# Optimization experiments

Hardware: AMD Instinct MI355X
Metric: run time of the kernel (lower is better)

Reference implementation:

```python
import jax, jax.numpy as jnp
import numpy as np

N_BINS = 50
FEATURE_ID = 0
EPS = 1e-7  # keras backend epsilon used by binary_crossentropy clipping


def setup_inputs() -> dict:
    key = jax.random.key(0)
    k1, k2 = jax.random.split(key)
    inputs = jax.random.normal(k1, (8_000_000, 4), dtype=jnp.float32)
    targets = jax.random.randint(k2, (8_000_000,), 0, 2, dtype=jnp.int32)
    return {"inputs": inputs, "targets": targets}


def _cut_forward(inputs, targets):
    # x: selected feature column, y: binary labels
    x = inputs[:, FEATURE_ID]
    y = targets
    N = x.shape[0]
    n_f = jnp.float32(N)

    x_min = jnp.min(x)
    x_max = jnp.max(x)
    E = N_BINS + 1
    edges = jnp.linspace(x_min, x_max, E)

    # Sort events once; prefix-sum of signal labels gives exact class counts
    # below/above any threshold (equivalent to the per-bin compare+count loop,
    # including the original's inclusive [lower, upper] double-counting of edges).
    order = jnp.argsort(x)
    xs = x[order]
    ys = (y[order] == 1).astype(jnp.float32)
    cs = jnp.concatenate([jnp.zeros((1,), jnp.float32), jnp.cumsum(ys)])  # [N+1]
    Ns = cs[-1]
    Nb = n_f - Ns

    r = jnp.searchsorted(xs, edges, side='right')  # count(x <= e)
    l = jnp.searchsorted(xs, edges, side='left')   # count(x <  e)
    ns_le = cs[r]
    ns_lt = cs[l]
    nb_le = r.astype(jnp.float32) - ns_le
    nb_lt = l.astype(jnp.float32) - ns_lt

    # hist[i] = count(lower[i] <= v <= upper[i]) per class
    hist0 = nb_le[1:] - nb_lt[:-1]  # background, [N_BINS]
    hist1 = ns_le[1:] - ns_lt[:-1]  # signal

    # candidate bin edges: sign-flip boundaries of hist0>hist1 with non-empty bins
    gt0 = hist0 > hist1
    cand0 = jnp.logical_xor(gt0[:-1], gt0[1:]) & (hist0[:-1] > 0)
    gt1 = hist1 > hist0
    cand1 = jnp.logical_xor(gt1[:-1], gt1[1:]) & (hist1[:-1] > 0)
    mask = jnp.zeros((E,), bool).at[1:N_BINS].set(cand0 | cand1)
    cnt = jnp.sum(mask)
    # original appends x_max when exactly one candidate survives
    mask = mask.at[-1].set(mask[-1] | (cnt == 1))

    # clipped BCE on hard 0/1 predictions reduces to a weighted error count:
    # correct sample -> -log(1-eps), wrong sample -> -log(eps)
    a = -jnp.log1p(jnp.float32(-EPS))
    b = -jnp.log(jnp.float32(EPS))

    def bce(correct):
        return ((n_f - correct) * b + correct * a) / n_f

    # per-edge losses for single-threshold cases
    c0 = ns_le + (Nb - nb_le)          # case 0: pred = (x <= c)
    c1 = (Ns - ns_lt) + nb_lt          # case 1: pred = (x >= c)
    # per-pair losses (i = lower cut, j = upper cut)
    c2 = (ns_le[None, :] - ns_lt[:, None]) + Nb - (nb_le[None, :] - nb_lt[:, None])
    c3 = ns_le[:, None] + (Ns - ns_lt[None, :]) + (nb_le[None, :] - nb_lt[:, None])

    L = jnp.stack([
        jnp.broadcast_to(bce(c0)[:, None], (E, E)),
        jnp.broadcast_to(bce(c1)[:, None], (E, E)),
        bce(c2),
        bce(c3),
    ])  # [4, E, E]
    per_pair_min = jnp.min(L, axis=0)
    per_pair_case = jnp.argmin(L, axis=0)

    idx = jnp.arange(E)
    valid = mask[:, None] & mask[None, :] & (idx[:, None] < idx[None, :])
    flat = jnp.argmin(jnp.where(valid, per_pair_min, jnp.inf))
    i = flat // E
    j = flat % E
    lower = edges[i]
    upper = edges[j]
    case = per_pair_case[i, j]

    pred0 = x <= lower
    pred1 = x >= lower
    pred2 = pred1 & (x <= upper)
    pred3 = pred0 | (x >= upper)
    y_pred = jnp.where(case == 0, pred0,
             jnp.where(case == 1, pred1,
             jnp.where(case == 2, pred2, pred3)))
    return y_pred


def reference(inputs, targets):
    return _cut_forward(inputs, targets).astype(jnp.int32)
```

## Files before the change

### kernel.cpp

```cpp
#include <hip/hip_runtime.h>
#include <math.h>
#include <stdint.h>

#define N_BINS 50
#define EDGE_N 51
#define HIST_N 52
#define NTHR 256
#define MAXBLK 2048
#define NREP 16

typedef unsigned int u32;
typedef unsigned short u16;
typedef unsigned char u8;
typedef float f32x4 __attribute__((ext_vector_type(4)));


#define KEEP16(v) asm volatile("" :: "v"(v))
#define ALOAD(p)     __hip_atomic_load((p), __ATOMIC_RELAXED, __HIP_MEMORY_SCOPE_AGENT)
#define ASTORE(p, v) __hip_atomic_store((p), (v), __ATOMIC_RELAXED, __HIP_MEMORY_SCOPE_AGENT)
#define AADD(p, v)   __hip_atomic_fetch_add((p), (v), __ATOMIC_RELAXED, __HIP_MEMORY_SCOPE_AGENT)
#define VDRAIN() asm volatile("s_waitcnt vmcnt(0)" ::: "memory")

__device__ __forceinline__ u32 f32_enc(float f) {
  u32 u = __float_as_uint(f);
  return (u & 0x80000000u) ? ~u : (u | 0x80000000u);
}
__device__ __forceinline__ float f32_dec(u32 k) {
  u32 u = (k & 0x80000000u) ? (k & 0x7fffffffu) : ~k;
  return __uint_as_float(u);
}
__device__ __forceinline__ u32* slot(u32* wsu, int base_b, int i) {
  return (u32*)((char*)wsu + base_b + i * 64);
}

__device__ __forceinline__ float edge_at(int e, float xmin, float xmax) {
  if (e >= N_BINS) return xmax;
  float step = __fdiv_rn((float)e, (float)N_BINS);
  float omst = __fsub_rn(1.0f, step);
  return __fadd_rn(__fmul_rn(xmin, omst), __fmul_rn(xmax, step));
}

__device__ __forceinline__ float bce_f(int c, float n_f, float aC, float bC) {
  float cf = (float)c;
  float t = __fadd_rn(__fmul_rn(__fsub_rn(n_f, cf), bC), __fmul_rn(cf, aC));
  return __fdiv_rn(t, n_f);
}

__device__ __forceinline__ void get_ab(float& aC, float& bC) {
  const double epsd = (double)1e-7f;
  aC = (float)(-log1p(-epsd));
  bC = (float)(-log(epsd));
}

__global__ void k_init(u32* __restrict__ wsu) {
  const int t = threadIdx.x;
  for (int i = t; i < 21376 / 4; i += NTHR) wsu[i] = 0u;
}

template <int COMPACT>
__global__ void __launch_bounds__(NTHR, 8)
k_all(const f32x4* __restrict__ in4, const int* __restrict__ tgt, int n, int nblk,
      u32* __restrict__ wsu, int* __restrict__ histU, int* __restrict__ histE,
      u32* __restrict__ bminArr, u32* __restrict__ bmaxArr,
      u8* __restrict__ codes, float* __restrict__ xc, int* __restrict__ out) {
  __shared__ int shU[2 * HIST_N];
  __shared__ float s_edges[EDGE_N];
  __shared__ int shE[2 * EDGE_N];
  __shared__ float s_red[8];
  __shared__ u32 s_redu[8];
  __shared__ float s_mm[2];
  __shared__ int s_ns_le[EDGE_N], s_ns_lt[EDGE_N], s_nb_le[EDGE_N], s_nb_lt[EDGE_N];
  __shared__ int s_h0[N_BINS], s_h1[N_BINS];
  __shared__ unsigned char s_g0[N_BINS], s_g1[N_BINS];
  __shared__ unsigned char s_mask[EDGE_N];
  __shared__ float s_rv[NTHR];
  __shared__ int s_ri[NTHR];
  __shared__ int s_cut[3];

  const int tid = threadIdx.x, bid = blockIdx.x;
  const int gid = bid * NTHR + tid;
  const int T = nblk * NTHR;
  const int rep = bid & (NREP - 1);

  for (int i = tid; i < 2 * HIST_N; i += NTHR) shU[i] = 0;
  for (int i = tid; i < 2 * EDGE_N; i += NTHR) shE[i] = 0;

  float vmin = INFINITY, vmax = -INFINITY;
#pragma unroll 4
  for (int i = gid; i < n; i += T) {
    f32x4 r = in4[i];
    KEEP16(r);
    float x = r.x;
    vmin = fminf(vmin, x);
    vmax = fmaxf(vmax, x);
    if (COMPACT) xc[i] = x;
  }
  for (int off = 32; off; off >>= 1) {
    vmin = fminf(vmin, __shfl_down(vmin, off));
    vmax = fmaxf(vmax, __shfl_down(vmax, off));
  }
  {
    int wid = tid >> 6;
    if ((tid & 63) == 0) { s_red[wid] = vmin; s_red[4 + wid] = vmax; }
  }
  __syncthreads();
  if (tid == 0) {
    float m = s_red[0], M = s_red[4];
    for (int w = 1; w < NTHR / 64; ++w) { m = fminf(m, s_red[w]); M = fmaxf(M, s_red[4 + w]); }
    ASTORE(&bminArr[bid], f32_enc(m));
    ASTORE(&bmaxArr[bid], f32_enc(M));
    VDRAIN();
    AADD(slot(wsu, 64, rep), 1u);
  }
  if (bid == 0) {
    if (tid == 0) {
      u32 s;
      do {
        s = 0;
#pragma unroll
        for (int k = 0; k < NREP; ++k) s += ALOAD(slot(wsu, 64, k));
        if (s < (u32)nblk) __builtin_amdgcn_s_sleep(8);
      } while (s < (u32)nblk);
    }
    __syncthreads();
    u32 eMin = 0xFFFFFFFFu, eMax = 0u;
    for (int i = tid; i < nblk; i += NTHR) {
      u32 a = ALOAD(&bminArr[i]);
      u32 b = ALOAD(&bmaxArr[i]);
      eMin = (a < eMin) ? a : eMin;
      eMax = (b > eMax) ? b : eMax;
    }
    for (int off = 32; off; off >>= 1) {
      u32 om = (u32)__shfl_down((int)eMin, off);
      u32 ox = (u32)__shfl_down((int)eMax, off);
      eMin = (om < eMin) ? om : eMin;
      eMax = (ox > eMax) ? ox : eMax;
    }
    {
      int wid = tid >> 6;
      if ((tid & 63) == 0) { s_redu[wid] = eMin; s_redu[4 + wid] = eMax; }
    }
    __syncthreads();
    if (tid == 0) {
      u32 mn = s_redu[0], mx = s_redu[4];
      for (int w = 1; w < NTHR / 64; ++w) {
        mn = (s_redu[w] < mn) ? s_redu[w] : mn;
        mx = (s_redu[4 + w] > mx) ? s_redu[4 + w] : mx;
      }
#pragma unroll
      for (int k = 0; k < NREP; ++k) {
        ASTORE(slot(wsu, 2112, k), mn);
        ASTORE(slot(wsu, 3136, k), mx);
      }
      VDRAIN();
#pragma unroll
      for (int k = 0; k < NREP; ++k) ASTORE(slot(wsu, 1088, k), 1u);
      s_mm[0] = f32_dec(mn);
      s_mm[1] = f32_dec(mx);
    }
  } else {
    if (tid == 0) {
      while (ALOAD(slot(wsu, 1088, rep)) == 0u) __builtin_amdgcn_s_sleep(64);
      s_mm[0] = f32_dec(ALOAD(slot(wsu, 2112, rep)));
      s_mm[1] = f32_dec(ALOAD(slot(wsu, 3136, rep)));
    }
  }
  __syncthreads();

  const float xmin = s_mm[0], xmax = s_mm[1];
  if (tid < EDGE_N) s_edges[tid] = edge_at(tid, xmin, xmax);
  __syncthreads();
  {
    const float delta = __fdiv_rn(__fsub_rn(xmax, xmin), (float)N_BINS);
    const float inv_delta = (delta > 0.0f) ? (1.0f / delta) : 0.0f;
    for (int i = gid; i < n; i += T) {
      float x;
      if (COMPACT) x = xc[i];
      else { f32x4 r = in4[i]; KEEP16(r); x = r.x; }
      int cls = (tgt[i] == 1) ? 0 : 1;
      int g = (int)((x - xmin) * inv_delta);
      g = max(0, min(g, EDGE_N));
      while (g < EDGE_N && s_edges[g] < x) ++g;
      while (g > 0 && s_edges[g - 1] >= x) --g;
      int eq = (g < EDGE_N && s_edges[g] == x) ? 1 : 0;
      atomicAdd(&shU[cls * HIST_N + g], 1);
      if (eq) atomicAdd(&shE[cls * EDGE_N + g], 1);
      if (COMPACT) codes[i] = (u8)(g | (eq << 6));
    }
    __syncthreads();
    int* hU = histU + rep * (2 * HIST_N);
    int* hE = histE + rep * (2 * EDGE_N);
    for (int kk = tid; kk < 2 * HIST_N; kk += NTHR) {
      int v = shU[kk];
      if (v) atomicAdd(&hU[kk], v);
    }
    for (int kk = tid; kk < 2 * EDGE_N; kk += NTHR) {
      int v = shE[kk];
      if (v) atomicAdd(&hE[kk], v);
    }
  }
  __syncthreads();
  if (tid == 0) {
    VDRAIN();
    AADD(slot(wsu, 4160, rep), 1u);
  }
  if (bid == 0) {
    if (tid == 0) {
      u32 s;
      do {
        s = 0;
#pragma unroll
        for (int k = 0; k < NREP; ++k) s += ALOAD(slot(wsu, 4160, k));
        if (s < (u32)nblk) __builtin_amdgcn_s_sleep(8);
      } while (s < (u32)nblk);
    }
    __syncthreads();
    if (tid < 128) {
      const int lane = tid & 63;
      const int w = tid >> 6;
      int v = 0;
      if (lane < EDGE_N) {
        for (int r = 0; r < NREP; ++r)
          v += ALOAD((u32*)&histU[r * (2 * HIST_N) + w * HIST_N + lane]);
      }
#pragma unroll
      for (int d = 1; d < 64; d <<= 1) {
        int t = __shfl_up(v, d);
        if (lane >= d) v += t;
      }
      if (lane < EDGE_N) {
        int e = 0;
        for (int r = 0; r < NREP; ++r)
          e += ALOAD((u32*)&histE[r * (2 * EDGE_N) + w * EDGE_N + lane]);
        if (w == 0) { s_ns_le[lane] = v; s_ns_lt[lane] = v - e; }
        else        { s_nb_le[lane] = v; s_nb_lt[lane] = v - e; }
      }
    }
    if (tid < EDGE_N) s_mask[tid] = 0;
    __syncthreads();
    if (tid < N_BINS) {
      int h0 = s_nb_le[tid + 1] - s_nb_lt[tid];
      int h1 = s_ns_le[tid + 1] - s_ns_lt[tid];
      s_h0[tid] = h0;
      s_h1[tid] = h1;
      s_g0[tid] = h0 > h1;
      s_g1[tid] = h1 > h0;
    }
    __syncthreads();
    if (tid < 64) {
      bool cand = false;
      if (tid + 1 < N_BINS) {
        bool c0 = (s_g0[tid] != s_g0[tid + 1]) && (s_h0[tid] > 0);
        bool c1 = (s_g1[tid] != s_g1[tid + 1]) && (s_h1[tid] > 0);
        cand = c0 || c1;
        if (cand) s_mask[tid + 1] = 1;
      }
      unsigned long long bal = __ballot(cand);
      if (tid == 0 && __popcll(bal) == 1) s_mask[N_BINS] = 1;
    }
    __syncthreads();
    const int Ns = s_ns_le[EDGE_N - 1];
    const int Nb = n - Ns;
    float aC, bC;
    get_ab(aC, bC);
    const float n_f = (float)n;
    float best = INFINITY;
    int bestIdx = 0x7fffffff;
    for (int p = tid; p < EDGE_N * EDGE_N; p += NTHR) {
      int i = p / EDGE_N, j = p - i * EDGE_N;
      float v = INFINITY;
      if (s_mask[i] && s_mask[j] && i < j) {
        int c0 = s_ns_le[i] + (Nb - s_nb_le[i]);
        int c1 = Ns - s_ns_lt[i] + s_nb_lt[i];
        int c2 = s_ns_le[j] - s_ns_lt[i] + Nb - (s_nb_le[j] - s_nb_lt[i]);
        int c3 = s_ns_le[i] + Ns - s_ns_lt[j] + s_nb_le[j] - s_nb_lt[i];
        float L0 = bce_f(c0, n_f, aC, bC);
        float L1 = bce_f(c1, n_f, aC, bC);
        float L2 = bce_f(c2, n_f, aC, bC);
        float L3 = bce_f(c3, n_f, aC, bC);
        v = L0;
        if (L1 < v) v = L1;
        if (L2 < v) v = L2;
        if (L3 < v) v = L3;
      }
      if (v < best || (v == best && p < bestIdx)) { best = v; bestIdx = p; }
    }
    s_rv[tid] = best;
    s_ri[tid] = bestIdx;
    __syncthreads();
    for (int s = NTHR / 2; s > 0; s >>= 1) {
      if (tid < s) {
        float ov = s_rv[tid + s];
        int oi = s_ri[tid + s];
        if (ov < s_rv[tid] || (ov == s_rv[tid] && oi < s_ri[tid])) {
          s_rv[tid] = ov;
          s_ri[tid] = oi;
        }
      }
      __syncthreads();
    }
    if (tid == 0) {
      int p = s_ri[0];
      int i = p / EDGE_N, j = p - i * EDGE_N;
      int c0 = s_ns_le[i] + (Nb - s_nb_le[i]);
      int c1 = Ns - s_ns_lt[i] + s_nb_lt[i];
      int c2 = s_ns_le[j] - s_ns_lt[i] + Nb - (s_nb_le[j] - s_nb_lt[i]);
      int c3 = s_ns_le[i] + Ns - s_ns_lt[j] + s_nb_le[j] - s_nb_lt[i];
      float L0 = bce_f(c0, n_f, aC, bC);
      float L1 = bce_f(c1, n_f, aC, bC);
      float L2 = bce_f(c2, n_f, aC, bC);
      float L3 = bce_f(c3, n_f, aC, bC);
      int cs = 0;
      float m = L0;
      if (L1 < m) { m = L1; cs = 1; }
      if (L2 < m) { m = L2; cs = 2; }
      if (L3 < m) { m = L3; cs = 3; }
      s_cut[0] = cs;
      s_cut[1] = i;
      s_cut[2] = j;
      u32 packed = 0x80000000u | ((u32)cs << 12) | ((u32)i << 6) | (u32)j;
#pragma unroll
      for (int k = 0; k < NREP; ++k) ASTORE(slot(wsu, 5184, k), packed);
    }
    __syncthreads();
  } else {
    if (tid == 0) {
      u32 f;
      while (((f = ALOAD(slot(wsu, 5184, rep))) & 0x80000000u) == 0u)
        __builtin_amdgcn_s_sleep(64);
      s_cut[0] = (int)((f >> 12) & 3u);
      s_cut[1] = (int)((f >> 6) & 63u);
      s_cut[2] = (int)(f & 63u);
    }
    __syncthreads();
  }

  const int cs = s_cut[0], ci = s_cut[1], cj = s_cut[2];
  if (COMPACT) {
    for (int i = gid; i < n; i += T) {
      u32 by = codes[i];
      int u = (int)(by & 63u);
      int v = u + (int)(by >> 6);
      bool p0 = (u <= ci), p1 = (ci < v);
      bool p = (cs == 0) ? p0 : (cs == 1) ? p1 : (cs == 2) ? (p1 && (u <= cj)) : (p0 || (cj < v));
      out[i] = p ? 1 : 0;
    }
  } else {
    const float lower = edge_at(ci, s_mm[0], s_mm[1]);
    const float upper = edge_at(cj, s_mm[0], s_mm[1]);
    for (int i = gid; i < n; i += T) {
      f32x4 r = in4[i];
      KEEP16(r);
      float x = r.x;
      bool p;
      if (cs == 0) p = (x <= lower);
      else if (cs == 1) p = (x >= lower);
      else if (cs == 2) p = (x >= lower) && (x <= upper);
      else p = (x <= lower) || (x >= upper);
      out[i] = p ? 1 : 0;
    }
  }
}

extern "C" void kernel_launch(void* const* d_in, const int* in_sizes, int n_in,
                              void* d_out, int out_size, void* d_ws, size_t ws_size,
                              hipStream_t stream) {
  const f32x4* in4 = (const f32x4*)d_in[0];
  const int* tgt = (const int*)d_in[1];
  int n = in_sizes[1];
  int* out = (int*)d_out;
  char* ws = (char*)d_ws;
  u32* wsu = (u32*)ws;
  int* histU = (int*)(ws + 8192);
  int* histE = (int*)(ws + 14848);
  u32* bminArr = (u32*)(ws + 21376);
  u32* bmaxArr = (u32*)(ws + 31616);
  u8* codes = (u8*)(ws + 49152);
  size_t xcOff = ((size_t)49152 + (size_t)n + 15) & ~(size_t)15;
  float* xc = (float*)(ws + xcOff);
  const bool compact = ws_size >= xcOff + (size_t)n * 4u;

  int maxb = 0;
  hipError_t oe = hipOccupancyMaxActiveBlocksPerMultiprocessor(
      &maxb, compact ? (const void*)k_all<1> : (const void*)k_all<0>, NTHR, 0);
  int nblk = MAXBLK;
  if (oe == hipSuccess && maxb > 0) {
    int cap = maxb * 256;
    if (cap < nblk) nblk = cap;
  } else {
    nblk = 1024;
  }

  k_init<<<1, NTHR, 0, stream>>>(wsu);
  void* args[12] = {(void*)&in4, (void*)&tgt, (void*)&n, (void*)&nblk, (void*)&wsu,
                    (void*)&histU, (void*)&histE, (void*)&bminArr, (void*)&bmaxArr,
                    (void*)&codes, (void*)&xc, (void*)&out};
  if (compact) {
    hipLaunchCooperativeKernel((void*)k_all<1>, dim3(nblk), dim3(NTHR), args, 0, stream);
  } else {
    hipLaunchCooperativeKernel((void*)k_all<0>, dim3(nblk), dim3(NTHR), args, 0, stream);
  }
}
```

Measured before the change: 87.29 us.

## Keep feature values and bin codes in registers across grid-sync phases

Adds a register-resident path (k_reg). With a fixed grid of 2048 blocks, each thread holds its 16 x values in registers and packs its bin codes into four u32 words. This removes the global writes and re-reads of the compacted x array and the byte-code array between phases. It also splits the shared histogram into one copy per wavefront to cut LDS atomic contention. The cost is higher register pressure, which could lower occupancy or break cooperative-launch residency, and the path only runs when n fits in 2048*256*16.

```diff
diff --git a/kernel.cpp b/kernel.cpp
--- a/kernel.cpp
+++ b/kernel.cpp
@@ -6,11 +6,11 @@
 #define EDGE_N 51
 #define HIST_N 52
 #define NTHR 256
-#define MAXBLK 2048
+#define RBLK 2048
+#define ITER 16
 #define NREP 16
 
 typedef unsigned int u32;
-typedef unsigned short u16;
 typedef unsigned char u8;
 typedef float f32x4 __attribute__((ext_vector_type(4)));
 
@@ -57,15 +57,127 @@
   for (int i = t; i < 21376 / 4; i += NTHR) wsu[i] = 0u;
 }
 
-template <int COMPACT>
+__device__ void decide_block0(int n, const int* __restrict__ histU,
+                              const int* __restrict__ histE, int* s_cut,
+                              int* s_ns_le, int* s_ns_lt, int* s_nb_le, int* s_nb_lt,
+                              int* s_h0, int* s_h1, unsigned char* s_g0,
+                              unsigned char* s_g1, unsigned char* s_mask,
+                              float* s_rv, int* s_ri) {
+  const int tid = threadIdx.x;
+  if (tid < 128) {
+    const int lane = tid & 63;
+    const int w = tid >> 6;
+    int v = 0;
+    if (lane < EDGE_N) {
+      for (int r = 0; r < NREP; ++r)
+        v += ALOAD((const u32*)&histU[r * (2 * HIST_N) + w * HIST_N + lane]);
+    }
+#pragma unroll
+    for (int d = 1; d < 64; d <<= 1) {
+      int t2 = __shfl_up(v, d);
+      if (lane >= d) v += t2;
+    }
+    if (lane < EDGE_N) {
+      int e = 0;
+      for (int r = 0; r < NREP; ++r)
+        e += ALOAD((const u32*)&histE[r * (2 * EDGE_N) + w * EDGE_N + lane]);
+      if (w == 0) { s_ns_le[lane] = v; s_ns_lt[lane] = v - e; }
+      else        { s_nb_le[lane] = v; s_nb_lt[lane] = v - e; }
+    }
+  }
+  if (tid < EDGE_N) s_mask[tid] = 0;
+  __syncthreads();
+  if (tid < N_BINS) {
+    int h0 = s_nb_le[tid + 1] - s_nb_lt[tid];
+    int h1 = s_ns_le[tid + 1] - s_ns_lt[tid];
+    s_h0[tid] = h0;
+    s_h1[tid] = h1;
+    s_g0[tid] = h0 > h1;
+    s_g1[tid] = h1 > h0;
+  }
+  __syncthreads();
+  if (tid < 64) {
+    bool cand = false;
+    if (tid + 1 < N_BINS) {
+      bool c0 = (s_g0[tid] != s_g0[tid + 1]) && (s_h0[tid] > 0);
+      bool c1 = (s_g1[tid] != s_g1[tid + 1]) && (s_h1[tid] > 0);
+      cand = c0 || c1;
+      if (cand) s_mask[tid + 1] = 1;
+    }
+    unsigned long long bal = __ballot(cand);
+    if (tid == 0 && __popcll(bal) == 1) s_mask[N_BINS] = 1;
+  }
+  __syncthreads();
+  const int Ns = s_ns_le[EDGE_N - 1];
+  const int Nb = n - Ns;
+  float aC, bC;
+  get_ab(aC, bC);
+  const float n_f = (float)n;
+  float best = INFINITY;
+  int bestIdx = 0x7fffffff;
+  for (int p = tid; p < EDGE_N * EDGE_N; p += NTHR) {
+    int i = p / EDGE_N, j = p - i * EDGE_N;
+    float v = INFINITY;
+    if (s_mask[i] && s_mask[j] && i < j) {
+      int c0 = s_ns_le[i] + (Nb - s_nb_le[i]);
+      int c1 = Ns - s_ns_lt[i] + s_nb_lt[i];
+      int c2 = s_ns_le[j] - s_ns_lt[i] + Nb - (s_nb_le[j] - s_nb_lt[i]);
+      int c3 = s_ns_le[i] + Ns - s_ns_lt[j] + s_nb_le[j] - s_nb_lt[i];
+      float L0 = bce_f(c0, n_f, aC, bC);
+      float L1 = bce_f(c1, n_f, aC, bC);
+      float L2 = bce_f(c2, n_f, aC, bC);
+      float L3 = bce_f(c3, n_f, aC, bC);
+      v = L0;
+      if (L1 < v) v = L1;
+      if (L2 < v) v = L2;
+      if (L3 < v) v = L3;
+    }
+    if (v < best || (v == best && p < bestIdx)) { best = v; bestIdx = p; }
+  }
+  s_rv[tid] = best;
+  s_ri[tid] = bestIdx;
+  __syncthreads();
+  for (int s = NTHR / 2; s > 0; s >>= 1) {
+    if (tid < s) {
+      float ov = s_rv[tid + s];
+      int oi = s_ri[tid + s];
+      if (ov < s_rv[tid] || (ov == s_rv[tid] && oi < s_ri[tid])) {
+        s_rv[tid] = ov;
+        s_ri[tid] = oi;
+      }
+    }
+    __syncthreads();
+  }
+  if (tid == 0) {
+    int p = s_ri[0];
+    int i = p / EDGE_N, j = p - i * EDGE_N;
+    int c0 = s_ns_le[i] + (Nb - s_nb_le[i]);
+    int c1 = Ns - s_ns_lt[i] + s_nb_lt[i];
+    int c2 = s_ns_le[j] - s_ns_lt[i] + Nb - (s_nb_le[j] - s_nb_lt[i]);
+    int c3 = s_ns_le[i] + Ns - s_ns_lt[j] + s_nb_le[j] - s_nb_lt[i];
+    float L0 = bce_f(c0, n_f, aC, bC);
+    float L1 = bce_f(c1, n_f, aC, bC);
+    float L2 = bce_f(c2, n_f, aC, bC);
+    float L3 = bce_f(c3, n_f, aC, bC);
+    int cs = 0;
+    float m = L0;
+    if (L1 < m) { m = L1; cs = 1; }
+    if (L2 < m) { m = L2; cs = 2; }
+    if (L3 < m) { m = L3; cs = 3; }
+    s_cut[0] = cs;
+    s_cut[1] = i;
+    s_cut[2] = j;
+  }
+  __syncthreads();
+}
+
 __global__ void __launch_bounds__(NTHR, 8)
-k_all(const f32x4* __restrict__ in4, const int* __restrict__ tgt, int n, int nblk,
+k_reg(const f32x4* __restrict__ in4, const int* __restrict__ tgt, int n,
       u32* __restrict__ wsu, int* __restrict__ histU, int* __restrict__ histE,
-      u32* __restrict__ bminArr, u32* __restrict__ bmaxArr,
-      u8* __restrict__ codes, float* __restrict__ xc, int* __restrict__ out) {
-  __shared__ int shU[2 * HIST_N];
+      u32* __restrict__ bminArr, u32* __restrict__ bmaxArr, int* __restrict__ out) {
+  __shared__ int shU[4][2 * HIST_N];
+  __shared__ int shE[2 * EDGE_N];
   __shared__ float s_edges[EDGE_N];
-  __shared__ int shE[2 * EDGE_N];
   __shared__ float s_red[8];
   __shared__ u32 s_redu[8];
   __shared__ float s_mm[2];
@@ -78,31 +190,33 @@
   __shared__ int s_cut[3];
 
   const int tid = threadIdx.x, bid = blockIdx.x;
+  const int wid = tid >> 6;
   const int gid = bid * NTHR + tid;
-  const int T = nblk * NTHR;
+  const int T = RBLK * NTHR;
   const int rep = bid & (NREP - 1);
 
-  for (int i = tid; i < 2 * HIST_N; i += NTHR) shU[i] = 0;
+  for (int i = tid; i < 4 * 2 * HIST_N; i += NTHR) ((int*)shU)[i] = 0;
   for (int i = tid; i < 2 * EDGE_N; i += NTHR) shE[i] = 0;
 
+  float xv[ITER];
   float vmin = INFINITY, vmax = -INFINITY;
-#pragma unroll 4
-  for (int i = gid; i < n; i += T) {
-    f32x4 r = in4[i];
-    KEEP16(r);
-    float x = r.x;
-    vmin = fminf(vmin, x);
-    vmax = fmaxf(vmax, x);
-    if (COMPACT) xc[i] = x;
+#pragma unroll
+  for (int k = 0; k < ITER; ++k) {
+    int i = gid + k * T;
+    xv[k] = 0.0f;
+    if (i < n) {
+      f32x4 r = in4[i];
+      KEEP16(r);
+      xv[k] = r.x;
+      vmin = fminf(vmin, xv[k]);
+      vmax = fmaxf(vmax, xv[k]);
+    }
   }
   for (int off = 32; off; off >>= 1) {
     vmin = fminf(vmin, __shfl_down(vmin, off));
     vmax = fmaxf(vmax, __shfl_down(vmax, off));
   }
-  {
-    int wid = tid >> 6;
-    if ((tid & 63) == 0) { s_red[wid] = vmin; s_red[4 + wid] = vmax; }
-  }
+  if ((tid & 63) == 0) { s_red[wid] = vmin; s_red[4 + wid] = vmax; }
   __syncthreads();
   if (tid == 0) {
     float m = s_red[0], M = s_red[4];
@@ -119,6 +233,196 @@
         s = 0;
 #pragma unroll
         for (int k = 0; k < NREP; ++k) s += ALOAD(slot(wsu, 64, k));
+        if (s < (u32)RBLK) __builtin_amdgcn_s_sleep(8);
+      } while (s < (u32)RBLK);
+    }
+    __syncthreads();
+    u32 eMin = 0xFFFFFFFFu, eMax = 0u;
+    for (int i = tid; i < RBLK; i += NTHR) {
+      u32 a = ALOAD(&bminArr[i]);
+      u32 b = ALOAD(&bmaxArr[i]);
+      eMin = (a < eMin) ? a : eMin;
+      eMax = (b > eMax) ? b : eMax;
+    }
+    for (int off = 32; off; off >>= 1) {
+      u32 om = (u32)__shfl_down((int)eMin, off);
+      u32 ox = (u32)__shfl_down((int)eMax, off);
+      eMin = (om < eMin) ? om : eMin;
+      eMax = (ox > eMax) ? ox : eMax;
+    }
+    if ((tid & 63) == 0) { s_redu[wid] = eMin; s_redu[4 + wid] = eMax; }
+    __syncthreads();
+    if (tid == 0) {
+      u32 mn = s_redu[0], mx = s_redu[4];
+      for (int w = 1; w < NTHR / 64; ++w) {
+        mn = (s_redu[w] < mn) ? s_redu[w] : mn;
+        mx = (s_redu[4 + w] > mx) ? s_redu[4 + w] : mx;
+      }
+#pragma unroll
+      for (int k = 0; k < NREP; ++k) {
+        ASTORE(slot(wsu, 2112, k), mn);
+        ASTORE(slot(wsu, 3136, k), mx);
+      }
+      VDRAIN();
+#pragma unroll
+      for (int k = 0; k < NREP; ++k) ASTORE(slot(wsu, 1088, k), 1u);
+      s_mm[0] = f32_dec(mn);
+      s_mm[1] = f32_dec(mx);
+    }
+  } else {
+    if (tid == 0) {
+      while (ALOAD(slot(wsu, 1088, rep)) == 0u) __builtin_amdgcn_s_sleep(64);
+      s_mm[0] = f32_dec(ALOAD(slot(wsu, 2112, rep)));
+      s_mm[1] = f32_dec(ALOAD(slot(wsu, 3136, rep)));
+    }
+  }
+  __syncthreads();
+
+  const float xmin = s_mm[0], xmax = s_mm[1];
+  if (tid < EDGE_N) s_edges[tid] = edge_at(tid, xmin, xmax);
+  __syncthreads();
+  u32 cw[ITER / 4] = {0, 0, 0, 0};
+  {
+    const float delta = __fdiv_rn(__fsub_rn(xmax, xmin), (float)N_BINS);
+    const float inv_delta = (delta > 0.0f) ? (1.0f / delta) : 0.0f;
+#pragma unroll
+    for (int k = 0; k < ITER; ++k) {
+      int i = gid + k * T;
+      if (i < n) {
+        float x = xv[k];
+        int cls = (tgt[i] == 1) ? 0 : 1;
+        int g = (int)((x - xmin) * inv_delta);
+        g = max(0, min(g, EDGE_N));
+        while (g < EDGE_N && s_edges[g] < x) ++g;
+        while (g > 0 && s_edges[g - 1] >= x) --g;
+        int eq = (g < EDGE_N && s_edges[g] == x) ? 1 : 0;
+        atomicAdd(&shU[wid][cls * HIST_N + g], 1);
+        if (eq) atomicAdd(&shE[cls * EDGE_N + g], 1);
+        cw[k >> 2] |= (u32)(g | (eq << 6)) << (8 * (k & 3));
+      }
+    }
+  }
+  __syncthreads();
+  {
+    int* hU = histU + rep * (2 * HIST_N);
+    int* hE = histE + rep * (2 * EDGE_N);
+    for (int kk = tid; kk < 2 * HIST_N; kk += NTHR) {
+      int v = shU[0][kk] + shU[1][kk] + shU[2][kk] + shU[3][kk];
+      if (v) atomicAdd(&hU[kk], v);
+    }
+    for (int kk = tid; kk < 2 * EDGE_N; kk += NTHR) {
+      int v = shE[kk];
+      if (v) atomicAdd(&hE[kk], v);
+    }
+  }
+  __syncthreads();
+  if (tid == 0) {
+    VDRAIN();
+    AADD(slot(wsu, 4160, rep), 1u);
+  }
+  if (bid == 0) {
+    if (tid == 0) {
+      u32 s;
+      do {
+        s = 0;
+#pragma unroll
+        for (int k = 0; k < NREP; ++k) s += ALOAD(slot(wsu, 4160, k));
+        if (s < (u32)RBLK) __builtin_amdgcn_s_sleep(8);
+      } while (s < (u32)RBLK);
+    }
+    __syncthreads();
+    decide_block0(n, histU, histE, s_cut, s_ns_le, s_ns_lt, s_nb_le, s_nb_lt,
+                  s_h0, s_h1, s_g0, s_g1, s_mask, s_rv, s_ri);
+    if (tid == 0) {
+      u32 packed = 0x80000000u | ((u32)s_cut[0] << 12) | ((u32)s_cut[1] << 6) | (u32)s_cut[2];
+#pragma unroll
+      for (int k = 0; k < NREP; ++k) ASTORE(slot(wsu, 5184, k), packed);
+    }
+    __syncthreads();
+  } else {
+    if (tid == 0) {
+      u32 f;
+      while (((f = ALOAD(slot(wsu, 5184, rep))) & 0x80000000u) == 0u)
+        __builtin_amdgcn_s_sleep(64);
+      s_cut[0] = (int)((f >> 12) & 3u);
+      s_cut[1] = (int)((f >> 6) & 63u);
+      s_cut[2] = (int)(f & 63u);
+    }
+    __syncthreads();
+  }
+
+  const int cs = s_cut[0], ci = s_cut[1], cj = s_cut[2];
+#pragma unroll
+  for (int k = 0; k < ITER; ++k) {
+    int i = gid + k * T;
+    if (i < n) {
+      u32 by = (cw[k >> 2] >> (8 * (k & 3))) & 0xFFu;
+      int u = (int)(by & 63u);
+      int v = u + (int)(by >> 6);
+      bool p0 = (u <= ci), p1 = (ci < v);
+      bool p = (cs == 0) ? p0 : (cs == 1) ? p1 : (cs == 2) ? (p1 && (u <= cj)) : (p0 || (cj < v));
+      out[i] = p ? 1 : 0;
+    }
+  }
+}
+
+__global__ void __launch_bounds__(NTHR, 8)
+k_ws(const f32x4* __restrict__ in4, const int* __restrict__ tgt, int n, int nblk,
+     u32* __restrict__ wsu, int* __restrict__ histU, int* __restrict__ histE,
+     u32* __restrict__ bminArr, u32* __restrict__ bmaxArr, int* __restrict__ out) {
+  __shared__ int shU[2 * HIST_N];
+  __shared__ int shE[2 * EDGE_N];
+  __shared__ float s_edges[EDGE_N];
+  __shared__ float s_red[8];
+  __shared__ u32 s_redu[8];
+  __shared__ float s_mm[2];
+  __shared__ int s_ns_le[EDGE_N], s_ns_lt[EDGE_N], s_nb_le[EDGE_N], s_nb_lt[EDGE_N];
+  __shared__ int s_h0[N_BINS], s_h1[N_BINS];
+  __shared__ unsigned char s_g0[N_BINS], s_g1[N_BINS];
+  __shared__ unsigned char s_mask[EDGE_N];
+  __shared__ float s_rv[NTHR];
+  __shared__ int s_ri[NTHR];
+  __shared__ int s_cut[3];
+
+  const int tid = threadIdx.x, bid = blockIdx.x;
+  const int gid = bid * NTHR + tid;
+  const int T = nblk * NTHR;
+  const int rep = bid & (NREP - 1);
+
+  for (int i = tid; i < 2 * HIST_N; i += NTHR) shU[i] = 0;
+  for (int i = tid; i < 2 * EDGE_N; i += NTHR) shE[i] = 0;
+
+  float vmin = INFINITY, vmax = -INFINITY;
+  for (int i = gid; i < n; i += T) {
+    f32x4 r = in4[i];
+    KEEP16(r);
+    vmin = fminf(vmin, r.x);
+    vmax = fmaxf(vmax, r.x);
+  }
+  for (int off = 32; off; off >>= 1) {
+    vmin = fminf(vmin, __shfl_down(vmin, off));
+    vmax = fmaxf(vmax, __shfl_down(vmax, off));
+  }
+  {
+    int wid = tid >> 6;
+    if ((tid & 63) == 0) { s_red[wid] = vmin; s_red[4 + wid] = vmax; }
+  }
+  __syncthreads();
+  if (tid == 0) {
+    float m = s_red[0], M = s_red[4];
+    for (int w = 1; w < NTHR / 64; ++w) { m = fminf(m, s_red[w]); M = fmaxf(M, s_red[4 + w]); }
+    ASTORE(&bminArr[bid], f32_enc(m));
+    ASTORE(&bmaxArr[bid], f32_enc(M));
+    VDRAIN();
+    AADD(slot(wsu, 64, rep), 1u);
+  }
+  if (bid == 0) {
+    if (tid == 0) {
+      u32 s;
+      do {
+        s = 0;
+#pragma unroll
+        for (int k = 0; k < NREP; ++k) s += ALOAD(slot(wsu, 64, k));
         if (s < (u32)nblk) __builtin_amdgcn_s_sleep(8);
       } while (s < (u32)nblk);
     }
@@ -166,7 +470,6 @@
     }
   }
   __syncthreads();
-
   const float xmin = s_mm[0], xmax = s_mm[1];
   if (tid < EDGE_N) s_edges[tid] = edge_at(tid, xmin, xmax);
   __syncthreads();
@@ -174,9 +477,9 @@
     const float delta = __fdiv_rn(__fsub_rn(xmax, xmin), (float)N_BINS);
     const float inv_delta = (delta > 0.0f) ? (1.0f / delta) : 0.0f;
     for (int i = gid; i < n; i += T) {
-      float x;
-      if (COMPACT) x = xc[i];
-      else { f32x4 r = in4[i]; KEEP16(r); x = r.x; }
+      f32x4 r = in4[i];
+      KEEP16(r);
+      float x = r.x;
       int cls = (tgt[i] == 1) ? 0 : 1;
       int g = (int)((x - xmin) * inv_delta);
       g = max(0, min(g, EDGE_N));
@@ -185,7 +488,6 @@
       int eq = (g < EDGE_N && s_edges[g] == x) ? 1 : 0;
       atomicAdd(&shU[cls * HIST_N + g], 1);
       if (eq) atomicAdd(&shE[cls * EDGE_N + g], 1);
-      if (COMPACT) codes[i] = (u8)(g | (eq << 6));
     }
     __syncthreads();
     int* hU = histU + rep * (2 * HIST_N);
@@ -215,110 +517,10 @@
       } while (s < (u32)nblk);
     }
     __syncthreads();
-    if (tid < 128) {
-      const int lane = tid & 63;
-      const int w = tid >> 6;
-      int v = 0;
-      if (lane < EDGE_N) {
-        for (int r = 0; r < NREP; ++r)
-          v += ALOAD((u32*)&histU[r * (2 * HIST_N) + w * HIST_N + lane]);
-      }
-#pragma unroll
-      for (int d = 1; d < 64; d <<= 1) {
-        int t = __shfl_up(v, d);
-        if (lane >= d) v += t;
-      }
-      if (lane < EDGE_N) {
-        int e = 0;
-        for (int r = 0; r < NREP; ++r)
-          e += ALOAD((u32*)&histE[r * (2 * EDGE_N) + w * EDGE_N + lane]);
-        if (w == 0) { s_ns_le[lane] = v; s_ns_lt[lane] = v - e; }
-        else        { s_nb_le[lane] = v; s_nb_lt[lane] = v - e; }
-      }
-    }
-    if (tid < EDGE_N) s_mask[tid] = 0;
-    __syncthreads();
-    if (tid < N_BINS) {
-      int h0 = s_nb_le[tid + 1] - s_nb_lt[tid];
-      int h1 = s_ns_le[tid + 1] - s_ns_lt[tid];
-      s_h0[tid] = h0;
-      s_h1[tid] = h1;
-      s_g0[tid] = h0 > h1;
-      s_g1[tid] = h1 > h0;
-    }
-    __syncthreads();
-    if (tid < 64) {
-      bool cand = false;
-      if (tid + 1 < N_BINS) {
-        bool c0 = (s_g0[tid] != s_g0[tid + 1]) && (s_h0[tid] > 0);
-        bool c1 = (s_g1[tid] != s_g1[tid + 1]) && (s_h1[tid] > 0);
-        cand = c0 || c1;
-        if (cand) s_mask[tid + 1] = 1;
-      }
-      unsigned long long bal = __ballot(cand);
-      if (tid == 0 && __popcll(bal) == 1) s_mask[N_BINS] = 1;
-    }
-    __syncthreads();
-    const int Ns = s_ns_le[EDGE_N - 1];
-    const int Nb = n - Ns;
-    float aC, bC;
-    get_ab(aC, bC);
-    const float n_f = (float)n;
-    float best = INFINITY;
-    int bestIdx = 0x7fffffff;
-    for (int p = tid; p < EDGE_N * EDGE_N; p += NTHR) {
-      int i = p / EDGE_N, j = p - i * EDGE_N;
-      float v = INFINITY;
-      if (s_mask[i] && s_mask[j] && i < j) {
-        int c0 = s_ns_le[i] + (Nb - s_nb_le[i]);
-        int c1 = Ns - s_ns_lt[i] + s_nb_lt[i];
-        int c2 = s_ns_le[j] - s_ns_lt[i] + Nb - (s_nb_le[j] - s_nb_lt[i]);
-        int c3 = s_ns_le[i] + Ns - s_ns_lt[j] + s_nb_le[j] - s_nb_lt[i];
-        float L0 = bce_f(c0, n_f, aC, bC);
-        float L1 = bce_f(c1, n_f, aC, bC);
-        float L2 = bce_f(c2, n_f, aC, bC);
-        float L3 = bce_f(c3, n_f, aC, bC);
-        v = L0;
-        if (L1 < v) v = L1;
-        if (L2 < v) v = L2;
-        if (L3 < v) v = L3;
-      }
-      if (v < best || (v == best && p < bestIdx)) { best = v; bestIdx = p; }
-    }
-    s_rv[tid] = best;
-    s_ri[tid] = bestIdx;
-    __syncthreads();
-    for (int s = NTHR / 2; s > 0; s >>= 1) {
-      if (tid < s) {
-        float ov = s_rv[tid + s];
-        int oi = s_ri[tid + s];
-        if (ov < s_rv[tid] || (ov == s_rv[tid] && oi < s_ri[tid])) {
-          s_rv[tid] = ov;
-          s_ri[tid] = oi;
-        }
-      }
-      __syncthreads();
-    }
-    if (tid == 0) {
-      int p = s_ri[0];
-      int i = p / EDGE_N, j = p - i * EDGE_N;
-      int c0 = s_ns_le[i] + (Nb - s_nb_le[i]);
-      int c1 = Ns - s_ns_lt[i] + s_nb_lt[i];
-      int c2 = s_ns_le[j] - s_ns_lt[i] + Nb - (s_nb_le[j] - s_nb_lt[i]);
-      int c3 = s_ns_le[i] + Ns - s_ns_lt[j] + s_nb_le[j] - s_nb_lt[i];
-      float L0 = bce_f(c0, n_f, aC, bC);
-      float L1 = bce_f(c1, n_f, aC, bC);
-      float L2 = bce_f(c2, n_f, aC, bC);
-      float L3 = bce_f(c3, n_f, aC, bC);
-      int cs = 0;
-      float m = L0;
-      if (L1 < m) { m = L1; cs = 1; }
-      if (L2 < m) { m = L2; cs = 2; }
-      if (L3 < m) { m = L3; cs = 3; }
-      s_cut[0] = cs;
-      s_cut[1] = i;
-      s_cut[2] = j;
-      u32 packed = 0x80000000u | ((u32)cs << 12) | ((u32)i << 6) | (u32)j;
+    decide_block0(n, histU, histE, s_cut, s_ns_le, s_ns_lt, s_nb_le, s_nb_lt,
+                  s_h0, s_h1, s_g0, s_g1, s_mask, s_rv, s_ri);
+    if (tid == 0) {
+      u32 packed = 0x80000000u | ((u32)s_cut[0] << 12) | ((u32)s_cut[1] << 6) | (u32)s_cut[2];
 #pragma unroll
       for (int k = 0; k < NREP; ++k) ASTORE(slot(wsu, 5184, k), packed);
     }
@@ -334,31 +536,19 @@
     }
     __syncthreads();
   }
-
   const int cs = s_cut[0], ci = s_cut[1], cj = s_cut[2];
-  if (COMPACT) {
-    for (int i = gid; i < n; i += T) {
-      u32 by = codes[i];
-      int u = (int)(by & 63u);
-      int v = u + (int)(by >> 6);
-      bool p0 = (u <= ci), p1 = (ci < v);
-      bool p = (cs == 0) ? p0 : (cs == 1) ? p1 : (cs == 2) ? (p1 && (u <= cj)) : (p0 || (cj < v));
-      out[i] = p ? 1 : 0;
-    }
-  } else {
-    const float lower = edge_at(ci, s_mm[0], s_mm[1]);
-    const float upper = edge_at(cj, s_mm[0], s_mm[1]);
-    for (int i = gid; i < n; i += T) {
-      f32x4 r = in4[i];
-      KEEP16(r);
-      float x = r.x;
-      bool p;
-      if (cs == 0) p = (x <= lower);
-      else if (cs == 1) p = (x >= lower);
-      else if (cs == 2) p = (x >= lower) && (x <= upper);
-      else p = (x <= lower) || (x >= upper);
-      out[i] = p ? 1 : 0;
-    }
+  const float lower = edge_at(ci, xmin, xmax);
+  const float upper = edge_at(cj, xmin, xmax);
+  for (int i = gid; i < n; i += T) {
+    f32x4 r = in4[i];
+    KEEP16(r);
+    float x = r.x;
+    bool p;
+    if (cs == 0) p = (x <= lower);
+    else if (cs == 1) p = (x >= lower);
+    else if (cs == 2) p = (x >= lower) && (x <= upper);
+    else p = (x <= lower) || (x >= upper);
+    out[i] = p ? 1 : 0;
   }
 }
 
@@ -375,29 +565,24 @@
   int* histE = (int*)(ws + 14848);
   u32* bminArr = (u32*)(ws + 21376);
   u32* bmaxArr = (u32*)(ws + 31616);
-  u8* codes = (u8*)(ws + 49152);
-  size_t xcOff = ((size_t)49152 + (size_t)n + 15) & ~(size_t)15;
-  float* xc = (float*)(ws + xcOff);
-  const bool compact = ws_size >= xcOff + (size_t)n * 4u;
 
   int maxb = 0;
-  hipError_t oe = hipOccupancyMaxActiveBlocksPerMultiprocessor(
-      &maxb, compact ? (const void*)k_all<1> : (const void*)k_all<0>, NTHR, 0);
-  int nblk = MAXBLK;
-  if (oe == hipSuccess && maxb > 0) {
-    int cap = maxb * 256;
-    if (cap < nblk) nblk = cap;
+  hipError_t oe = hipOccupancyMaxActiveBlocksPerMultiprocessor(&maxb, (const void*)k_reg, NTHR, 0);
+  const bool regOK = (oe == hipSuccess) && (maxb * 256 >= RBLK) &&
+                     ((long long)n <= (long long)RBLK * NTHR * ITER);
+
+  k_init<<<1, NTHR, 0, stream>>>(wsu);
+  if (regOK) {
+    void* args[9] = {(void*)&in4, (void*)&tgt, (void*)&n, (void*)&wsu,
+                     (void*)&histU, (void*)&histE, (void*)&bminArr, (void*)&bmaxArr,
+                     (void*)&out};
+    hipLaunchCooperativeKernel((void*)k_reg, dim3(RBLK), dim3(NTHR), args, 0, stream);
   } else {
-    nblk = 1024;
-  }
-
-  k_init<<<1, NTHR, 0, stream>>>(wsu);
-  void* args[12] = {(void*)&in4, (void*)&tgt, (void*)&n, (void*)&nblk, (void*)&wsu,
-                    (void*)&histU, (void*)&histE, (void*)&bminArr, (void*)&bmaxArr,
-                    (void*)&codes, (void*)&xc, (void*)&out};
-  if (compact) {
-    hipLaunchCooperativeKernel((void*)k_all<1>, dim3(nblk), dim3(NTHR), args, 0, stream);
-  } else {
-    hipLaunchCooperativeKernel((void*)k_all<0>, dim3(nblk), dim3(NTHR), args, 0, stream);
-  }
-}
+    int nblk = (maxb > 0) ? maxb * 256 : 1024;
+    if (nblk > 2048) nblk = 2048;
+    void* args[10] = {(void*)&in4, (void*)&tgt, (void*)&n, (void*)&nblk, (void*)&wsu,
+                      (void*)&histU, (void*)&histE, (void*)&bminArr, (void*)&bmaxArr,
+                      (void*)&out};
+    hipLaunchCooperativeKernel((void*)k_ws, dim3(nblk), dim3(NTHR), args, 0, stream);
+  }
+}
```

Measured after the change: 107.3 us. 1.23x slower.
